# Performance work log

Measured on AMD Instinct MI355X. Metric: run time of the kernel, lower is better.

## Reference

```python
import jax, jax.numpy as jnp
import numpy as np

N, B, D, K, H = 30000, 16, 32, 8, 8
DIST = 5.0
EPS = 1e-6


def setup_inputs() -> dict:
    key = jax.random.key(0)
    ks = jax.random.split(key, 16)
    sc = 1.0 / np.sqrt(D)
    inp = {
        'pos': jax.random.uniform(ks[0], (N, 3), jnp.float32) * 20.0,
        'node_features': jax.random.normal(ks[1], (N, D), jnp.float32),
        'batch': jnp.sort(jax.random.randint(ks[2], (N,), 0, B, dtype=jnp.int32)),
        'bessel_weights': jnp.linspace(jnp.pi, K * jnp.pi, K).astype(jnp.float32),
        'init_dummy': jax.random.normal(ks[3], (D,), jnp.float32),
        'Wq_dummy': jax.random.normal(ks[4], (D, D), jnp.float32) * sc,
        'Wq_graph': jax.random.normal(ks[5], (D, D), jnp.float32) * sc,
        'Wdot': jax.random.normal(ks[6], (D, D), jnp.float32) * sc,
        'W1_kd': jax.random.normal(ks[7], (K, H), jnp.float32) / np.sqrt(K),
        'W2_kd': jax.random.normal(ks[8], (H, D * D), jnp.float32) / np.sqrt(H),
        'W1_vd': jax.random.normal(ks[9], (K, H), jnp.float32) / np.sqrt(K),
        'W2_vd': jax.random.normal(ks[10], (H, D * D), jnp.float32) / np.sqrt(H),
        'W1_kg': jax.random.normal(ks[11], (K, H), jnp.float32) / np.sqrt(K),
        'W2_kg': jax.random.normal(ks[12], (H, D * D), jnp.float32) / np.sqrt(H),
        'W1_vg': jax.random.normal(ks[13], (K, H), jnp.float32) / np.sqrt(K),
        'W2_vg': jax.random.normal(ks[14], (H, D * D), jnp.float32) / np.sqrt(H),
    }
    return inp


def reference(pos, node_features, batch, bessel_weights, init_dummy,
              Wq_dummy, Wq_graph, Wdot,
              W1_kd, W2_kd, W1_vd, W2_vd, W1_kg, W2_kg, W1_vg, W2_vg):
    scale = 1.0 / np.sqrt(D)

    # --- dummy edge features: per-batch z extents + bessel basis ---
    z = pos[:, 2]                                            # [N]
    z_min = jax.ops.segment_min(z, batch, num_segments=B)    # [B]
    z_max = jax.ops.segment_max(z, batch, num_segments=B)    # [B]
    bot_len = z - z_min[batch] + DIST                        # [N]
    top_len = z_max[batch] + DIST - z                        # [N]

    def bessel(x):  # [N] -> [N,K]
        return jnp.sin(bessel_weights * x[:, None]) / (x[:, None] + EPS)

    edge = jnp.stack([bessel(bot_len), bessel(top_len)], axis=1)  # [N,2,K]

    # --- init dummy node features [B, 2, D] ---
    dummy = jnp.broadcast_to(init_dummy, (B, 2, D))

    def gen_w(W1, W2):  # conditional weight generator (silu MLP)
        return (jax.nn.silu(edge @ W1) @ W2).reshape(N, 2, D, D)

    # --- dummy nodes attend over graph nodes (segment softmax) ---
    wk = gen_w(W1_kd, W2_kd)                                 # [N,2,D,D]
    wv = gen_w(W1_vd, W2_vd)
    q = (dummy @ Wq_dummy)[batch]                            # [N,2,D]
    k = jnp.einsum('nd,nsde->nse', node_features, wk)        # [N,2,D]
    v = jnp.einsum('nd,nsde->nse', node_features, wv)
    s = jnp.einsum('nsq,qk,nsk->ns', q, Wdot, k) * scale     # [N,2]
    m = jax.ops.segment_max(s, batch, num_segments=B)
    e = jnp.exp(s - m[batch])
    zsum = jax.ops.segment_sum(e, batch, num_segments=B)
    attn = e / zsum[batch]                                   # [N,2]
    dummy_new = dummy + jax.ops.segment_sum(attn[..., None] * v, batch, num_segments=B)

    # --- graph nodes attend over (2) dummy nodes ---
    wkg = gen_w(W1_kg, W2_kg)
    wvg = gen_w(W1_vg, W2_vg)
    d_per = dummy_new[batch]                                 # [N,2,D]
    kg = jnp.einsum('nsd,nsde->nse', d_per, wkg)
    vg = jnp.einsum('nsd,nsde->nse', d_per, wvg)
    qg = node_features @ Wq_graph                            # [N,D]
    sg = jnp.einsum('nq,qk,nsk->ns', qg, Wdot, kg) * scale   # [N,2]
    ag = jax.nn.softmax(sg, axis=1)
    x_new = node_features + jnp.einsum('ns,nsd->nd', ag, vg)  # [N,D]
    return x_new
```

## Files before the change

kernel.cpp:

```cpp
#include <hip/hip_runtime.h>
#include <math.h>

#define NN 30000
#define BB 16
#define DD 32
#define KK 8
#define HH 8
#define DIST_C 5.0f
#define EPS_C 1e-6f
#define SCALE_C 0.17677669529663687f

#define WS_ZMIN 0
#define WS_ZMAX 16
#define WS_ZSUM 32
#define WS_QW   64
#define WS_PK   96
#define WS_WC   352
#define WS_T    1376
#define WS_AKG  9568
#define WS_AVG  17760

#define NPB 32

__device__ __forceinline__ unsigned fencode(float f) {
    unsigned u = __float_as_uint(f);
    return (u & 0x80000000u) ? ~u : (u | 0x80000000u);
}
__device__ __forceinline__ float fdecode(unsigned c) {
    return __uint_as_float((c & 0x80000000u) ? (c ^ 0x80000000u) : ~c);
}
__device__ __forceinline__ float silu(float x) { return x / (1.0f + expf(-x)); }

__device__ __forceinline__ void bessel_edges(float bw0, float x0, float x1, float edge[2][8]) {
    float xs[2]; xs[0] = x0; xs[1] = x1;
    #pragma unroll
    for (int s = 0; s < 2; ++s) {
        float x = xs[s];
        float inv = 1.0f / (x + EPS_C);
        float th = bw0 * x;
        float c2 = 2.0f * cosf(th);
        float skm1 = 0.0f;
        float sk = sinf(th);
        #pragma unroll
        for (int k = 0; k < 8; ++k) {
            edge[s][k] = sk * inv;
            float nx = c2 * sk - skm1;
            skm1 = sk;
            sk = nx;
        }
    }
}

__global__ __launch_bounds__(256) void k_init(const float* __restrict__ init_dummy,
                                              const float* __restrict__ Wq_dummy,
                                              const float* __restrict__ Wdot,
                                              const float* __restrict__ W2_kd,
                                              const float* __restrict__ Wq_graph,
                                              float* __restrict__ ws) {
    __shared__ float qvec[32];
    __shared__ float qWl[32];
    int t = threadIdx.x;
    unsigned* wsu = (unsigned*)ws;
    if (t < 16) { wsu[WS_ZMIN + t] = 0xFFFFFFFFu; wsu[WS_ZMAX + t] = 0u; }
    if (t < 32) ws[WS_ZSUM + t] = 0.0f;
    for (int i = t; i < 8192; i += 256) ws[WS_T + i] = 0.0f;
    if (t < 32) {
        float acc = 0.0f;
        for (int d = 0; d < 32; ++d) acc += init_dummy[d] * Wq_dummy[d * 32 + t];
        qvec[t] = acc;
    }
    __syncthreads();
    if (t < 32) {
        float acc = 0.0f;
        for (int e = 0; e < 32; ++e) acc += qvec[e] * Wdot[e * 32 + t];
        qWl[t] = acc;
        ws[WS_QW + t] = acc;
    }
    __syncthreads();
    {
        int h = t >> 5, d = t & 31;
        float acc = 0.0f;
        for (int e = 0; e < 32; ++e) acc += W2_kd[h * 1024 + d * 32 + e] * qWl[e];
        ws[WS_PK + t] = acc;
    }
    for (int i = t; i < 1024; i += 256) {
        int d = i >> 5, e = i & 31;
        float acc = 0.0f;
        for (int m = 0; m < 32; ++m) acc += Wq_graph[d * 32 + m] * Wdot[m * 32 + e];
        ws[WS_WC + i] = acc;
    }
}

__global__ __launch_bounds__(256) void k_zminmax(const float* __restrict__ pos,
                                                 const int* __restrict__ batch,
                                                 float* __restrict__ ws) {
    __shared__ unsigned zl[16], zh[16];
    int t = threadIdx.x;
    if (t < 16) { zl[t] = 0xFFFFFFFFu; zh[t] = 0u; }
    __syncthreads();
    int n = blockIdx.x * 256 + t;
    if (n < NN) {
        unsigned c = fencode(pos[3 * n + 2]);
        int b = batch[n];
        atomicMin(&zl[b], c);
        atomicMax(&zh[b], c);
    }
    __syncthreads();
    unsigned* wsu = (unsigned*)ws;
    if (t < 16) {
        if (zl[t] != 0xFFFFFFFFu) atomicMin(&wsu[WS_ZMIN + t], zl[t]);
        if (zh[t] != 0u)          atomicMax(&wsu[WS_ZMAX + t], zh[t]);
    }
}

__global__ __launch_bounds__(256) void k_phase1(const float* __restrict__ pos,
                                                const int* __restrict__ batch,
                                                const float* __restrict__ nf,
                                                const float* __restrict__ bw,
                                                const float* __restrict__ W1_kd,
                                                const float* __restrict__ W1_vd,
                                                float* __restrict__ ws) {
    __shared__ __align__(16) float Fl[NPB * 36];
    __shared__ float Lw[NPB * 17];
    __shared__ int   Lb[NPB];
    __shared__ __align__(16) float Pk[256];
    __shared__ float W1kd[64], W1vd[64], zsl[32];
    int t = threadIdx.x;
    if (t < 64) { W1kd[t] = W1_kd[t]; W1vd[t] = W1_vd[t]; }
    Pk[t] = ws[WS_PK + t];
    if (t < 32) zsl[t] = 0.0f;

    int li = t >> 3, g = t & 7;
    int n0 = blockIdx.x * NPB;
    int n = n0 + li;
    bool valid = n < NN;
    float4 fv4 = make_float4(0.f, 0.f, 0.f, 0.f);
    int b = 0;
    if (valid) {
        b = batch[n];
        fv4 = ((const float4*)nf)[n * 8 + g];
        ((float4*)(Fl + li * 36))[g] = fv4;
        if (g == 0) Lb[li] = b;
    } else {
        if (g == 0) Lb[li] = -1;
    }
    __syncthreads();

    if (valid) {
        const unsigned* wsu = (const unsigned*)ws;
        float z = pos[3 * n + 2];
        float zmin = fdecode(wsu[WS_ZMIN + b]);
        float zmax = fdecode(wsu[WS_ZMAX + b]);
        float edge[2][8];
        bessel_edges(bw[0], z - zmin + DIST_C, zmax + DIST_C - z, edge);

        float up[8];
        const float4* Pk4 = (const float4*)Pk;
        #pragma unroll
        for (int h = 0; h < 8; ++h) {
            float4 p = Pk4[h * 8 + g];
            up[h] = fv4.x * p.x + fv4.y * p.y + fv4.z * p.z + fv4.w * p.w;
        }
        float kd0, kd1;
        {
            float p0 = 0.f, p1 = 0.f;
            #pragma unroll
            for (int k = 0; k < 8; ++k) {
                float w = W1kd[k * 8 + g];
                p0 += edge[0][k] * w;
                p1 += edge[1][k] * w;
            }
            kd0 = silu(p0); kd1 = silu(p1);
        }
        int lanebase = (t & 63) & 56;
        float sp0 = 0.f, sp1 = 0.f;
        #pragma unroll
        for (int h = 0; h < 8; ++h) {
            float a0 = __shfl(kd0, lanebase + h, 64);
            float a1 = __shfl(kd1, lanebase + h, 64);
            sp0 += a0 * up[h];
            sp1 += a1 * up[h];
        }
        #pragma unroll
        for (int m = 1; m < 8; m <<= 1) {
            sp0 += __shfl_xor(sp0, m, 64);
            sp1 += __shfl_xor(sp1, m, 64);
        }
        float ev0 = expf(sp0 * SCALE_C);
        float ev1 = expf(sp1 * SCALE_C);
        if (g == 0) {
            atomicAdd(&zsl[b * 2 + 0], ev0);
            atomicAdd(&zsl[b * 2 + 1], ev1);
        }
        float q0 = 0.f, q1 = 0.f;
        #pragma unroll
        for (int k = 0; k < 8; ++k) {
            float w = W1vd[k * 8 + g];
            q0 += edge[0][k] * w;
            q1 += edge[1][k] * w;
        }
        Lw[li * 17 + g]     = ev0 * silu(q0);
        Lw[li * 17 + 8 + g] = ev1 * silu(q1);
    }
    __syncthreads();
    if (t < 32 && zsl[t] != 0.0f) atomicAdd(&ws[WS_ZSUM + t], zsl[t]);

    int count = NN - n0; if (count > NPB) count = NPB;
    int bf = Lb[0], bl = Lb[count - 1];
    int sh = t & 15, dp = t >> 4;
    for (int b2 = bf; b2 <= bl; ++b2) {
        float a0 = 0.f, a1 = 0.f;
        for (int i = 0; i < count; ++i) {
            if (Lb[i] != b2) continue;
            float w = Lw[i * 17 + sh];
            float2 x = *(const float2*)(Fl + i * 36 + 2 * dp);
            a0 += w * x.x;
            a1 += w * x.y;
        }
        float* Tb = ws + WS_T + b2 * 512 + sh * 32 + 2 * dp;
        atomicAdd(&Tb[0], a0);
        atomicAdd(&Tb[1], a1);
    }
}

__global__ __launch_bounds__(256) void k_batch(const float* __restrict__ init_dummy,
                                               const float* __restrict__ W2_vd,
                                               const float* __restrict__ W2_kg,
                                               const float* __restrict__ W2_vg,
                                               float* __restrict__ ws) {
    int bs = blockIdx.x;
    int b = bs >> 1, s = bs & 1;
    int t = threadIdx.x;
    __shared__ float Tl[256];
    __shared__ float part[256];
    __shared__ float dn[32];
    Tl[t] = ws[WS_T + b * 512 + s * 256 + t];
    __syncthreads();
    {
        int h = t >> 5, e = t & 31;
        float acc = 0.0f;
        #pragma unroll
        for (int d = 0; d < 32; ++d) acc += Tl[h * 32 + d] * W2_vd[h * 1024 + d * 32 + e];
        part[t] = acc;
    }
    __syncthreads();
    if (t < 32) {
        float acc = 0.0f;
        #pragma unroll
        for (int h = 0; h < 8; ++h) acc += part[h * 32 + t];
        float zs = ws[WS_ZSUM + b * 2 + s];
        dn[t] = init_dummy[t] + acc / zs;
    }
    __syncthreads();
    {
        int h = t >> 5, e = t & 31;
        float ak = 0.0f, av = 0.0f;
        #pragma unroll
        for (int d = 0; d < 32; ++d) {
            float dv = dn[d];
            ak += dv * W2_kg[h * 1024 + d * 32 + e];
            av += dv * W2_vg[h * 1024 + d * 32 + e];
        }
        ws[WS_AKG + b * 512 + s * 256 + t] = ak;
        ws[WS_AVG + b * 512 + s * 256 + t] = av;
    }
}

__global__ __launch_bounds__(256) void k_final(const float* __restrict__ pos,
                                               const int* __restrict__ batch,
                                               const float* __restrict__ nf,
                                               const float* __restrict__ bw,
                                               const float* __restrict__ W1_kg,
                                               const float* __restrict__ W1_vg,
                                               const float* __restrict__ ws,
                                               float* __restrict__ out) {
    __shared__ __align__(16) float Wc[1024];
    __shared__ __align__(16) float Fl[NPB * 36];
    __shared__ float W1kg[64], W1vg[64];
    int t = threadIdx.x;
    for (int i = t; i < 1024; i += 256) Wc[i] = ws[WS_WC + i];
    if (t < 64) { W1kg[t] = W1_kg[t]; W1vg[t] = W1_vg[t]; }

    int li = t >> 3, g = t & 7;
    int n0 = blockIdx.x * NPB;
    int n = n0 + li;
    bool valid = n < NN;
    float4 fv4 = make_float4(0.f, 0.f, 0.f, 0.f);
    if (valid) {
        fv4 = ((const float4*)nf)[n * 8 + g];
        ((float4*)(Fl + li * 36))[g] = fv4;
    }
    __syncthreads();
    if (!valid) return;

    int b = batch[n];
    const unsigned* wsu = (const unsigned*)ws;
    float z = pos[3 * n + 2];
    float zmin = fdecode(wsu[WS_ZMIN + b]);
    float zmax = fdecode(wsu[WS_ZMAX + b]);
    float edge[2][8];
    bessel_edges(bw[0], z - zmin + DIST_C, zmax + DIST_C - z, edge);

    float ak0, ak1, av0, av1;
    {
        float pk0 = 0.f, pk1 = 0.f, pv0 = 0.f, pv1 = 0.f;
        #pragma unroll
        for (int k = 0; k < 8; ++k) {
            float wk = W1kg[k * 8 + g];
            float wv = W1vg[k * 8 + g];
            pk0 += edge[0][k] * wk; pk1 += edge[1][k] * wk;
            pv0 += edge[0][k] * wv; pv1 += edge[1][k] * wv;
        }
        ak0 = silu(pk0); ak1 = silu(pk1);
        av0 = silu(pv0); av1 = silu(pv1);
    }

    float f[32];
    {
        const float4* myF4 = (const float4*)(Fl + li * 36);
        #pragma unroll
        for (int j = 0; j < 8; ++j) {
            float4 v = myF4[j];
            f[4 * j] = v.x; f[4 * j + 1] = v.y; f[4 * j + 2] = v.z; f[4 * j + 3] = v.w;
        }
    }
    float4 q4 = make_float4(0.f, 0.f, 0.f, 0.f);
    const float4* Wc4 = (const float4*)Wc;
    #pragma unroll
    for (int d = 0; d < 32; ++d) {
        float fd = f[d];
        float4 w = Wc4[d * 8 + g];
        q4.x += fd * w.x; q4.y += fd * w.y; q4.z += fd * w.z; q4.w += fd * w.w;
    }

    int lanebase = (t & 63) & 56;
    const float4* Ak4 = (const float4*)(ws + WS_AKG);
    const float4* Av4 = (const float4*)(ws + WS_AVG);
    float p0 = 0.f, p1 = 0.f;
    #pragma unroll
    for (int h = 0; h < 8; ++h) {
        float4 a0 = Ak4[b * 128 + h * 8 + g];
        float4 a1 = Ak4[b * 128 + 64 + h * 8 + g];
        float d0 = q4.x * a0.x + q4.y * a0.y + q4.z * a0.z + q4.w * a0.w;
        float d1 = q4.x * a1.x + q4.y * a1.y + q4.z * a1.z + q4.w * a1.w;
        p0 += __shfl(ak0, lanebase + h, 64) * d0;
        p1 += __shfl(ak1, lanebase + h, 64) * d1;
    }
    #pragma unroll
    for (int m = 1; m < 8; m <<= 1) {
        p0 += __shfl_xor(p0, m, 64);
        p1 += __shfl_xor(p1, m, 64);
    }
    float sg0 = p0 * SCALE_C, sg1 = p1 * SCALE_C;
    float mm = fmaxf(sg0, sg1);
    float e0 = expf(sg0 - mm), e1 = expf(sg1 - mm);
    float inv = 1.0f / (e0 + e1);
    float ag0 = e0 * inv, ag1 = e1 * inv;

    float4 x4 = fv4;
    #pragma unroll
    for (int h = 0; h < 8; ++h) {
        float w0 = ag0 * __shfl(av0, lanebase + h, 64);
        float w1 = ag1 * __shfl(av1, lanebase + h, 64);
        float4 a0 = Av4[b * 128 + h * 8 + g];
        float4 a1 = Av4[b * 128 + 64 + h * 8 + g];
        x4.x += w0 * a0.x + w1 * a1.x;
        x4.y += w0 * a0.y + w1 * a1.y;
        x4.z += w0 * a0.z + w1 * a1.z;
        x4.w += w0 * a0.w + w1 * a1.w;
    }
    ((float4*)out)[n * 8 + g] = x4;
}

extern "C" void kernel_launch(void* const* d_in, const int* in_sizes, int n_in,
                              void* d_out, int out_size, void* d_ws, size_t ws_size,
                              hipStream_t stream) {
    const float* pos        = (const float*)d_in[0];
    const float* nf         = (const float*)d_in[1];
    const int*   batch      = (const int*)d_in[2];
    const float* bw         = (const float*)d_in[3];
    const float* init_dummy = (const float*)d_in[4];
    const float* Wq_dummy   = (const float*)d_in[5];
    const float* Wq_graph   = (const float*)d_in[6];
    const float* Wdot       = (const float*)d_in[7];
    const float* W1_kd      = (const float*)d_in[8];
    const float* W2_kd      = (const float*)d_in[9];
    const float* W1_vd      = (const float*)d_in[10];
    const float* W2_vd      = (const float*)d_in[11];
    const float* W1_kg      = (const float*)d_in[12];
    const float* W2_kg      = (const float*)d_in[13];
    const float* W1_vg      = (const float*)d_in[14];
    const float* W2_vg      = (const float*)d_in[15];
    float* ws  = (float*)d_ws;
    float* out = (float*)d_out;

    int nblk1 = (NN + 255) / 256;
    int nblk8 = (NN + NPB - 1) / NPB;
    hipLaunchKernelGGL(k_init, dim3(1), dim3(256), 0, stream,
                       init_dummy, Wq_dummy, Wdot, W2_kd, Wq_graph, ws);
    hipLaunchKernelGGL(k_zminmax, dim3(nblk1), dim3(256), 0, stream, pos, batch, ws);
    hipLaunchKernelGGL(k_phase1, dim3(nblk8), dim3(256), 0, stream,
                       pos, batch, nf, bw, W1_kd, W1_vd, ws);
    hipLaunchKernelGGL(k_batch, dim3(32), dim3(256), 0, stream,
                       init_dummy, W2_vd, W2_kg, W2_vg, ws);
    hipLaunchKernelGGL(k_final, dim3(nblk8), dim3(256), 0, stream,
                       pos, batch, nf, bw, W1_kg, W1_vg, ws, out);
}
```

Baseline: 124.3 us.

## Fuse five kernels into one cooperative persistent kernel with grid syncs

Replaces the five separate launches (init, z min/max, phase1, per-batch, final) with a single cooperative kernel of 469 blocks, each handling two 32-node tiles, separated by grid-wide syncs. Node features, z, batch ids and bessel edges are computed once per block and kept in registers and shared memory across phases instead of being reloaded. The z min/max reduction now writes per-block partials that 16 blocks reduce, replacing global atomics. A multi-launch fallback using mode flags remains for when cooperative launch is unavailable. The cost is four grid barriers and higher register and LDS pressure per block.

```diff
diff --git a/kernel.cpp b/kernel.cpp
--- a/kernel.cpp
+++ b/kernel.cpp
@@ -1,26 +1,35 @@
 #include <hip/hip_runtime.h>
+#include <hip/hip_cooperative_groups.h>
 #include <math.h>
+
+namespace cg = cooperative_groups;
 
 #define NN 30000
 #define BB 16
-#define DD 32
-#define KK 8
-#define HH 8
 #define DIST_C 5.0f
 #define EPS_C 1e-6f
 #define SCALE_C 0.17677669529663687f
 
-#define WS_ZMIN 0
-#define WS_ZMAX 16
-#define WS_ZSUM 32
-#define WS_QW   64
-#define WS_PK   96
-#define WS_WC   352
-#define WS_T    1376
-#define WS_AKG  9568
-#define WS_AVG  17760
-
 #define NPB 32
+#define TPB 2
+#define GRID 469
+
+#define WS_ZMIN  0
+#define WS_ZMAX  16
+#define WS_ZSUM  32
+#define WS_PK    96
+#define WS_WC    352
+#define WS_T     1376
+#define WS_AKG   9568
+#define WS_AVG   17760
+#define WS_ZPART 25952
+
+#define M_PRE 1
+#define M_RED 2
+#define M_A   4
+#define M_B   8
+#define M_C   16
+#define M_ALL 31
 
 __device__ __forceinline__ unsigned fencode(float f) {
     unsigned u = __float_as_uint(f);
@@ -51,325 +60,317 @@
     }
 }
 
-__global__ __launch_bounds__(256) void k_init(const float* __restrict__ init_dummy,
-                                              const float* __restrict__ Wq_dummy,
-                                              const float* __restrict__ Wdot,
-                                              const float* __restrict__ W2_kd,
-                                              const float* __restrict__ Wq_graph,
-                                              float* __restrict__ ws) {
-    __shared__ float qvec[32];
-    __shared__ float qWl[32];
+__global__ __launch_bounds__(256, 2) void k_main(
+    const float* __restrict__ pos, const int* __restrict__ batch,
+    const float* __restrict__ nf, const float* __restrict__ bw,
+    const float* __restrict__ W1_kd, const float* __restrict__ W1_vd,
+    const float* __restrict__ W1_kg, const float* __restrict__ W1_vg,
+    const float* __restrict__ init_dummy, const float* __restrict__ Wq_dummy,
+    const float* __restrict__ Wdot, const float* __restrict__ W2_kd,
+    const float* __restrict__ W2_vd, const float* __restrict__ W2_kg,
+    const float* __restrict__ W2_vg, const float* __restrict__ Wq_graph,
+    float* __restrict__ ws, float* __restrict__ out, int mode)
+{
+    __shared__ __align__(16) float Fl[TPB][NPB * 36];
+    __shared__ float Lw[TPB][NPB * 17];
+    __shared__ int   Lb[TPB][NPB];
+    __shared__ __align__(16) float Pk[256];
+    __shared__ __align__(16) float Wc[1024];
+    __shared__ float W1kd[64], W1vd[64], W1kg[64], W1vg[64], zsl[32];
+    __shared__ unsigned zl[16], zh[16];
+    __shared__ float qvec[32], qWl[32];
+    __shared__ float Tl[256], part[256], dn[32];
+
+    const bool coop   = (mode == M_ALL);
+    const bool do_pre = mode & M_PRE;
+    const bool do_red = mode & M_RED;
+    const bool do_a   = mode & M_A;
+    const bool do_b   = mode & M_B;
+    const bool do_c   = mode & M_C;
+
     int t = threadIdx.x;
+    int li = t >> 3, g = t & 7;
+    int lanebase = (t & 63) & 56;
     unsigned* wsu = (unsigned*)ws;
-    if (t < 16) { wsu[WS_ZMIN + t] = 0xFFFFFFFFu; wsu[WS_ZMAX + t] = 0u; }
-    if (t < 32) ws[WS_ZSUM + t] = 0.0f;
-    for (int i = t; i < 8192; i += 256) ws[WS_T + i] = 0.0f;
-    if (t < 32) {
-        float acc = 0.0f;
-        for (int d = 0; d < 32; ++d) acc += init_dummy[d] * Wq_dummy[d * 32 + t];
-        qvec[t] = acc;
-    }
-    __syncthreads();
-    if (t < 32) {
-        float acc = 0.0f;
-        for (int e = 0; e < 32; ++e) acc += qvec[e] * Wdot[e * 32 + t];
-        qWl[t] = acc;
-        ws[WS_QW + t] = acc;
-    }
-    __syncthreads();
-    {
-        int h = t >> 5, d = t & 31;
-        float acc = 0.0f;
-        for (int e = 0; e < 32; ++e) acc += W2_kd[h * 1024 + d * 32 + e] * qWl[e];
-        ws[WS_PK + t] = acc;
-    }
-    for (int i = t; i < 1024; i += 256) {
-        int d = i >> 5, e = i & 31;
-        float acc = 0.0f;
-        for (int m = 0; m < 32; ++m) acc += Wq_graph[d * 32 + m] * Wdot[m * 32 + e];
-        ws[WS_WC + i] = acc;
-    }
-}
-
-__global__ __launch_bounds__(256) void k_zminmax(const float* __restrict__ pos,
-                                                 const int* __restrict__ batch,
-                                                 float* __restrict__ ws) {
-    __shared__ unsigned zl[16], zh[16];
-    int t = threadIdx.x;
-    if (t < 16) { zl[t] = 0xFFFFFFFFu; zh[t] = 0u; }
-    __syncthreads();
-    int n = blockIdx.x * 256 + t;
-    if (n < NN) {
-        unsigned c = fencode(pos[3 * n + 2]);
-        int b = batch[n];
-        atomicMin(&zl[b], c);
-        atomicMax(&zh[b], c);
-    }
-    __syncthreads();
-    unsigned* wsu = (unsigned*)ws;
-    if (t < 16) {
-        if (zl[t] != 0xFFFFFFFFu) atomicMin(&wsu[WS_ZMIN + t], zl[t]);
-        if (zh[t] != 0u)          atomicMax(&wsu[WS_ZMAX + t], zh[t]);
-    }
-}
-
-__global__ __launch_bounds__(256) void k_phase1(const float* __restrict__ pos,
-                                                const int* __restrict__ batch,
-                                                const float* __restrict__ nf,
-                                                const float* __restrict__ bw,
-                                                const float* __restrict__ W1_kd,
-                                                const float* __restrict__ W1_vd,
-                                                float* __restrict__ ws) {
-    __shared__ __align__(16) float Fl[NPB * 36];
-    __shared__ float Lw[NPB * 17];
-    __shared__ int   Lb[NPB];
-    __shared__ __align__(16) float Pk[256];
-    __shared__ float W1kd[64], W1vd[64], zsl[32];
-    int t = threadIdx.x;
-    if (t < 64) { W1kd[t] = W1_kd[t]; W1vd[t] = W1_vd[t]; }
-    Pk[t] = ws[WS_PK + t];
-    if (t < 32) zsl[t] = 0.0f;
-
-    int li = t >> 3, g = t & 7;
-    int n0 = blockIdx.x * NPB;
-    int n = n0 + li;
-    bool valid = n < NN;
-    float4 fv4 = make_float4(0.f, 0.f, 0.f, 0.f);
-    int b = 0;
-    if (valid) {
-        b = batch[n];
-        fv4 = ((const float4*)nf)[n * 8 + g];
-        ((float4*)(Fl + li * 36))[g] = fv4;
-        if (g == 0) Lb[li] = b;
-    } else {
-        if (g == 0) Lb[li] = -1;
-    }
-    __syncthreads();
-
-    if (valid) {
-        const unsigned* wsu = (const unsigned*)ws;
-        float z = pos[3 * n + 2];
-        float zmin = fdecode(wsu[WS_ZMIN + b]);
-        float zmax = fdecode(wsu[WS_ZMAX + b]);
-        float edge[2][8];
-        bessel_edges(bw[0], z - zmin + DIST_C, zmax + DIST_C - z, edge);
-
-        float up[8];
-        const float4* Pk4 = (const float4*)Pk;
-        #pragma unroll
-        for (int h = 0; h < 8; ++h) {
-            float4 p = Pk4[h * 8 + g];
-            up[h] = fv4.x * p.x + fv4.y * p.y + fv4.z * p.z + fv4.w * p.w;
-        }
-        float kd0, kd1;
+
+    float4 fv4[TPB]; float zreg[TPB]; int bseg[TPB]; bool val[TPB];
+    float bw0 = 0.f;
+    if (do_pre || do_a || do_c) {
+        bw0 = bw[0];
+        #pragma unroll
+        for (int it = 0; it < TPB; ++it) {
+            int n = (blockIdx.x * TPB + it) * NPB + li;
+            val[it] = (n < NN);
+            bseg[it] = 0; zreg[it] = 0.f;
+            fv4[it] = make_float4(0.f, 0.f, 0.f, 0.f);
+            if (val[it]) {
+                bseg[it] = batch[n];
+                fv4[it] = ((const float4*)nf)[n * 8 + g];
+                ((float4*)(Fl[it] + li * 36))[g] = fv4[it];
+                zreg[it] = pos[3 * n + 2];
+                if (g == 0) Lb[it][li] = bseg[it];
+            } else if (g == 0) Lb[it][li] = -1;
+        }
+    }
+
+    if (do_pre) {
+        if (t < 16) { zl[t] = 0xFFFFFFFFu; zh[t] = 0u; }
+        __syncthreads();
+        #pragma unroll
+        for (int it = 0; it < TPB; ++it)
+            if (val[it] && g == 0) {
+                unsigned c = fencode(zreg[it]);
+                atomicMin(&zl[bseg[it]], c);
+                atomicMax(&zh[bseg[it]], c);
+            }
+        __syncthreads();
+        if (t < 16) {
+            wsu[WS_ZPART + blockIdx.x * 32 + t]      = zl[t];
+            wsu[WS_ZPART + blockIdx.x * 32 + 16 + t] = zh[t];
+        }
+        int xb = blockIdx.x;
+        if (xb >= 32 && xb < 48) {
+            int off = (xb - 32) * 512 + t;
+            ws[WS_T + off] = 0.f; ws[WS_T + off + 256] = 0.f;
+        } else if (xb == 48) {
+            if (t < 32) ws[WS_ZSUM + t] = 0.f;
+        } else if (xb == 49) {
+            if (t < 32) {
+                float acc = 0.f;
+                for (int d = 0; d < 32; ++d) acc += init_dummy[d] * Wq_dummy[d * 32 + t];
+                qvec[t] = acc;
+            }
+            __syncthreads();
+            if (t < 32) {
+                float acc = 0.f;
+                for (int e = 0; e < 32; ++e) acc += qvec[e] * Wdot[e * 32 + t];
+                qWl[t] = acc;
+            }
+            __syncthreads();
+            {
+                int h = t >> 5, d = t & 31;
+                float acc = 0.f;
+                for (int e = 0; e < 32; ++e) acc += W2_kd[h * 1024 + d * 32 + e] * qWl[e];
+                ws[WS_PK + t] = acc;
+            }
+        } else if (xb >= 50 && xb < 54) {
+            int i = (xb - 50) * 256 + t;
+            int d = i >> 5, e = i & 31;
+            float acc = 0.f;
+            for (int m = 0; m < 32; ++m) acc += Wq_graph[d * 32 + m] * Wdot[m * 32 + e];
+            ws[WS_WC + i] = acc;
+        }
+    }
+    if (coop) cg::this_grid().sync();
+
+    if (do_red && blockIdx.x < 16) {
+        int b = blockIdx.x;
+        unsigned mn = 0xFFFFFFFFu, mx = 0u;
+        for (int e = t; e < GRID; e += 256) {
+            unsigned a = wsu[WS_ZPART + e * 32 + b];
+            unsigned c = wsu[WS_ZPART + e * 32 + 16 + b];
+            mn = (a < mn) ? a : mn;
+            mx = (c > mx) ? c : mx;
+        }
+        if (t == 0) { zl[0] = 0xFFFFFFFFu; zh[0] = 0u; }
+        __syncthreads();
+        atomicMin(&zl[0], mn);
+        atomicMax(&zh[0], mx);
+        __syncthreads();
+        if (t == 0) { wsu[WS_ZMIN + b] = zl[0]; wsu[WS_ZMAX + b] = zh[0]; }
+    }
+    if (coop) cg::this_grid().sync();
+
+    float edge[TPB][2][8];
+    if (do_a || do_c) {
+        Pk[t] = ws[WS_PK + t];
+        for (int i = t; i < 1024; i += 256) Wc[i] = ws[WS_WC + i];
+        if (t < 64) { W1kd[t] = W1_kd[t]; W1vd[t] = W1_vd[t]; W1kg[t] = W1_kg[t]; W1vg[t] = W1_vg[t]; }
+        if (t < 32) zsl[t] = 0.f;
+        __syncthreads();
+        #pragma unroll
+        for (int it = 0; it < TPB; ++it)
+            if (val[it]) {
+                float zmin = fdecode(wsu[WS_ZMIN + bseg[it]]);
+                float zmax = fdecode(wsu[WS_ZMAX + bseg[it]]);
+                bessel_edges(bw0, zreg[it] - zmin + DIST_C, zmax + DIST_C - zreg[it], edge[it]);
+            }
+    }
+
+    if (do_a) {
+        #pragma unroll
+        for (int it = 0; it < TPB; ++it) {
+            if (val[it]) {
+                float up[8];
+                const float4* Pk4 = (const float4*)Pk;
+                #pragma unroll
+                for (int h = 0; h < 8; ++h) {
+                    float4 p = Pk4[h * 8 + g];
+                    up[h] = fv4[it].x * p.x + fv4[it].y * p.y + fv4[it].z * p.z + fv4[it].w * p.w;
+                }
+                float p0 = 0.f, p1 = 0.f;
+                #pragma unroll
+                for (int k = 0; k < 8; ++k) {
+                    float w = W1kd[k * 8 + g];
+                    p0 += edge[it][0][k] * w;
+                    p1 += edge[it][1][k] * w;
+                }
+                float kd0 = silu(p0), kd1 = silu(p1);
+                float sp0 = 0.f, sp1 = 0.f;
+                #pragma unroll
+                for (int h = 0; h < 8; ++h) {
+                    sp0 += __shfl(kd0, lanebase + h, 64) * up[h];
+                    sp1 += __shfl(kd1, lanebase + h, 64) * up[h];
+                }
+                #pragma unroll
+                for (int m = 1; m < 8; m <<= 1) {
+                    sp0 += __shfl_xor(sp0, m, 64);
+                    sp1 += __shfl_xor(sp1, m, 64);
+                }
+                float ev0 = expf(sp0 * SCALE_C);
+                float ev1 = expf(sp1 * SCALE_C);
+                if (g == 0) {
+                    atomicAdd(&zsl[bseg[it] * 2 + 0], ev0);
+                    atomicAdd(&zsl[bseg[it] * 2 + 1], ev1);
+                }
+                float q0 = 0.f, q1 = 0.f;
+                #pragma unroll
+                for (int k = 0; k < 8; ++k) {
+                    float w = W1vd[k * 8 + g];
+                    q0 += edge[it][0][k] * w;
+                    q1 += edge[it][1][k] * w;
+                }
+                Lw[it][li * 17 + g]     = ev0 * silu(q0);
+                Lw[it][li * 17 + 8 + g] = ev1 * silu(q1);
+            }
+        }
+        __syncthreads();
+        if (t < 32 && zsl[t] != 0.f) atomicAdd(&ws[WS_ZSUM + t], zsl[t]);
+        #pragma unroll
+        for (int it = 0; it < TPB; ++it) {
+            int n0 = (blockIdx.x * TPB + it) * NPB;
+            int count = NN - n0; if (count > NPB) count = NPB;
+            int bf = Lb[it][0], bl = Lb[it][count - 1];
+            int sh = t & 15, dp = t >> 4;
+            for (int b2 = bf; b2 <= bl; ++b2) {
+                float a0 = 0.f, a1 = 0.f;
+                for (int i = 0; i < count; ++i) {
+                    if (Lb[it][i] != b2) continue;
+                    float w = Lw[it][i * 17 + sh];
+                    float2 x = *(const float2*)(Fl[it] + i * 36 + 2 * dp);
+                    a0 += w * x.x;
+                    a1 += w * x.y;
+                }
+                float* Tb = ws + WS_T + b2 * 512 + sh * 32 + 2 * dp;
+                atomicAdd(&Tb[0], a0);
+                atomicAdd(&Tb[1], a1);
+            }
+        }
+    }
+    if (coop) cg::this_grid().sync();
+
+    if (do_b && blockIdx.x < 32) {
+        int bb = blockIdx.x >> 1, s = blockIdx.x & 1;
+        Tl[t] = ws[WS_T + bb * 512 + s * 256 + t];
+        __syncthreads();
         {
-            float p0 = 0.f, p1 = 0.f;
+            int h = t >> 5, e = t & 31;
+            float acc = 0.f;
             #pragma unroll
-            for (int k = 0; k < 8; ++k) {
-                float w = W1kd[k * 8 + g];
-                p0 += edge[0][k] * w;
-                p1 += edge[1][k] * w;
-            }
-            kd0 = silu(p0); kd1 = silu(p1);
-        }
-        int lanebase = (t & 63) & 56;
-        float sp0 = 0.f, sp1 = 0.f;
-        #pragma unroll
-        for (int h = 0; h < 8; ++h) {
-            float a0 = __shfl(kd0, lanebase + h, 64);
-            float a1 = __shfl(kd1, lanebase + h, 64);
-            sp0 += a0 * up[h];
-            sp1 += a1 * up[h];
-        }
-        #pragma unroll
-        for (int m = 1; m < 8; m <<= 1) {
-            sp0 += __shfl_xor(sp0, m, 64);
-            sp1 += __shfl_xor(sp1, m, 64);
-        }
-        float ev0 = expf(sp0 * SCALE_C);
-        float ev1 = expf(sp1 * SCALE_C);
-        if (g == 0) {
-            atomicAdd(&zsl[b * 2 + 0], ev0);
-            atomicAdd(&zsl[b * 2 + 1], ev1);
-        }
-        float q0 = 0.f, q1 = 0.f;
-        #pragma unroll
-        for (int k = 0; k < 8; ++k) {
-            float w = W1vd[k * 8 + g];
-            q0 += edge[0][k] * w;
-            q1 += edge[1][k] * w;
-        }
-        Lw[li * 17 + g]     = ev0 * silu(q0);
-        Lw[li * 17 + 8 + g] = ev1 * silu(q1);
-    }
-    __syncthreads();
-    if (t < 32 && zsl[t] != 0.0f) atomicAdd(&ws[WS_ZSUM + t], zsl[t]);
-
-    int count = NN - n0; if (count > NPB) count = NPB;
-    int bf = Lb[0], bl = Lb[count - 1];
-    int sh = t & 15, dp = t >> 4;
-    for (int b2 = bf; b2 <= bl; ++b2) {
-        float a0 = 0.f, a1 = 0.f;
-        for (int i = 0; i < count; ++i) {
-            if (Lb[i] != b2) continue;
-            float w = Lw[i * 17 + sh];
-            float2 x = *(const float2*)(Fl + i * 36 + 2 * dp);
-            a0 += w * x.x;
-            a1 += w * x.y;
-        }
-        float* Tb = ws + WS_T + b2 * 512 + sh * 32 + 2 * dp;
-        atomicAdd(&Tb[0], a0);
-        atomicAdd(&Tb[1], a1);
-    }
-}
-
-__global__ __launch_bounds__(256) void k_batch(const float* __restrict__ init_dummy,
-                                               const float* __restrict__ W2_vd,
-                                               const float* __restrict__ W2_kg,
-                                               const float* __restrict__ W2_vg,
-                                               float* __restrict__ ws) {
-    int bs = blockIdx.x;
-    int b = bs >> 1, s = bs & 1;
-    int t = threadIdx.x;
-    __shared__ float Tl[256];
-    __shared__ float part[256];
-    __shared__ float dn[32];
-    Tl[t] = ws[WS_T + b * 512 + s * 256 + t];
-    __syncthreads();
-    {
-        int h = t >> 5, e = t & 31;
-        float acc = 0.0f;
-        #pragma unroll
-        for (int d = 0; d < 32; ++d) acc += Tl[h * 32 + d] * W2_vd[h * 1024 + d * 32 + e];
-        part[t] = acc;
-    }
-    __syncthreads();
-    if (t < 32) {
-        float acc = 0.0f;
-        #pragma unroll
-        for (int h = 0; h < 8; ++h) acc += part[h * 32 + t];
-        float zs = ws[WS_ZSUM + b * 2 + s];
-        dn[t] = init_dummy[t] + acc / zs;
-    }
-    __syncthreads();
-    {
-        int h = t >> 5, e = t & 31;
-        float ak = 0.0f, av = 0.0f;
-        #pragma unroll
-        for (int d = 0; d < 32; ++d) {
-            float dv = dn[d];
-            ak += dv * W2_kg[h * 1024 + d * 32 + e];
-            av += dv * W2_vg[h * 1024 + d * 32 + e];
-        }
-        ws[WS_AKG + b * 512 + s * 256 + t] = ak;
-        ws[WS_AVG + b * 512 + s * 256 + t] = av;
-    }
-}
-
-__global__ __launch_bounds__(256) void k_final(const float* __restrict__ pos,
-                                               const int* __restrict__ batch,
-                                               const float* __restrict__ nf,
-                                               const float* __restrict__ bw,
-                                               const float* __restrict__ W1_kg,
-                                               const float* __restrict__ W1_vg,
-                                               const float* __restrict__ ws,
-                                               float* __restrict__ out) {
-    __shared__ __align__(16) float Wc[1024];
-    __shared__ __align__(16) float Fl[NPB * 36];
-    __shared__ float W1kg[64], W1vg[64];
-    int t = threadIdx.x;
-    for (int i = t; i < 1024; i += 256) Wc[i] = ws[WS_WC + i];
-    if (t < 64) { W1kg[t] = W1_kg[t]; W1vg[t] = W1_vg[t]; }
-
-    int li = t >> 3, g = t & 7;
-    int n0 = blockIdx.x * NPB;
-    int n = n0 + li;
-    bool valid = n < NN;
-    float4 fv4 = make_float4(0.f, 0.f, 0.f, 0.f);
-    if (valid) {
-        fv4 = ((const float4*)nf)[n * 8 + g];
-        ((float4*)(Fl + li * 36))[g] = fv4;
-    }
-    __syncthreads();
-    if (!valid) return;
-
-    int b = batch[n];
-    const unsigned* wsu = (const unsigned*)ws;
-    float z = pos[3 * n + 2];
-    float zmin = fdecode(wsu[WS_ZMIN + b]);
-    float zmax = fdecode(wsu[WS_ZMAX + b]);
-    float edge[2][8];
-    bessel_edges(bw[0], z - zmin + DIST_C, zmax + DIST_C - z, edge);
-
-    float ak0, ak1, av0, av1;
-    {
-        float pk0 = 0.f, pk1 = 0.f, pv0 = 0.f, pv1 = 0.f;
-        #pragma unroll
-        for (int k = 0; k < 8; ++k) {
-            float wk = W1kg[k * 8 + g];
-            float wv = W1vg[k * 8 + g];
-            pk0 += edge[0][k] * wk; pk1 += edge[1][k] * wk;
-            pv0 += edge[0][k] * wv; pv1 += edge[1][k] * wv;
-        }
-        ak0 = silu(pk0); ak1 = silu(pk1);
-        av0 = silu(pv0); av1 = silu(pv1);
-    }
-
-    float f[32];
-    {
-        const float4* myF4 = (const float4*)(Fl + li * 36);
-        #pragma unroll
-        for (int j = 0; j < 8; ++j) {
-            float4 v = myF4[j];
-            f[4 * j] = v.x; f[4 * j + 1] = v.y; f[4 * j + 2] = v.z; f[4 * j + 3] = v.w;
-        }
-    }
-    float4 q4 = make_float4(0.f, 0.f, 0.f, 0.f);
-    const float4* Wc4 = (const float4*)Wc;
-    #pragma unroll
-    for (int d = 0; d < 32; ++d) {
-        float fd = f[d];
-        float4 w = Wc4[d * 8 + g];
-        q4.x += fd * w.x; q4.y += fd * w.y; q4.z += fd * w.z; q4.w += fd * w.w;
-    }
-
-    int lanebase = (t & 63) & 56;
-    const float4* Ak4 = (const float4*)(ws + WS_AKG);
-    const float4* Av4 = (const float4*)(ws + WS_AVG);
-    float p0 = 0.f, p1 = 0.f;
-    #pragma unroll
-    for (int h = 0; h < 8; ++h) {
-        float4 a0 = Ak4[b * 128 + h * 8 + g];
-        float4 a1 = Ak4[b * 128 + 64 + h * 8 + g];
-        float d0 = q4.x * a0.x + q4.y * a0.y + q4.z * a0.z + q4.w * a0.w;
-        float d1 = q4.x * a1.x + q4.y * a1.y + q4.z * a1.z + q4.w * a1.w;
-        p0 += __shfl(ak0, lanebase + h, 64) * d0;
-        p1 += __shfl(ak1, lanebase + h, 64) * d1;
-    }
-    #pragma unroll
-    for (int m = 1; m < 8; m <<= 1) {
-        p0 += __shfl_xor(p0, m, 64);
-        p1 += __shfl_xor(p1, m, 64);
-    }
-    float sg0 = p0 * SCALE_C, sg1 = p1 * SCALE_C;
-    float mm = fmaxf(sg0, sg1);
-    float e0 = expf(sg0 - mm), e1 = expf(sg1 - mm);
-    float inv = 1.0f / (e0 + e1);
-    float ag0 = e0 * inv, ag1 = e1 * inv;
-
-    float4 x4 = fv4;
-    #pragma unroll
-    for (int h = 0; h < 8; ++h) {
-        float w0 = ag0 * __shfl(av0, lanebase + h, 64);
-        float w1 = ag1 * __shfl(av1, lanebase + h, 64);
-        float4 a0 = Av4[b * 128 + h * 8 + g];
-        float4 a1 = Av4[b * 128 + 64 + h * 8 + g];
-        x4.x += w0 * a0.x + w1 * a1.x;
-        x4.y += w0 * a0.y + w1 * a1.y;
-        x4.z += w0 * a0.z + w1 * a1.z;
-        x4.w += w0 * a0.w + w1 * a1.w;
-    }
-    ((float4*)out)[n * 8 + g] = x4;
+            for (int d = 0; d < 32; ++d) acc += Tl[h * 32 + d] * W2_vd[h * 1024 + d * 32 + e];
+            part[t] = acc;
+        }
+        __syncthreads();
+        if (t < 32) {
+            float acc = 0.f;
+            #pragma unroll
+            for (int h = 0; h < 8; ++h) acc += part[h * 32 + t];
+            float zs = ws[WS_ZSUM + bb * 2 + s];
+            dn[t] = init_dummy[t] + acc / zs;
+        }
+        __syncthreads();
+        {
+            int h = t >> 5, e = t & 31;
+            float ak = 0.f, av = 0.f;
+            #pragma unroll
+            for (int d = 0; d < 32; ++d) {
+                float dv = dn[d];
+                ak += dv * W2_kg[h * 1024 + d * 32 + e];
+                av += dv * W2_vg[h * 1024 + d * 32 + e];
+            }
+            ws[WS_AKG + bb * 512 + s * 256 + t] = ak;
+            ws[WS_AVG + bb * 512 + s * 256 + t] = av;
+        }
+    }
+    if (coop) cg::this_grid().sync();
+
+    if (do_c) {
+        const float4* Ak4 = (const float4*)(ws + WS_AKG);
+        const float4* Av4 = (const float4*)(ws + WS_AVG);
+        const float4* Wc4 = (const float4*)Wc;
+        #pragma unroll
+        for (int it = 0; it < TPB; ++it) {
+            if (val[it]) {
+                int b = bseg[it];
+                float ak0, ak1, av0, av1;
+                {
+                    float pk0 = 0.f, pk1 = 0.f, pv0 = 0.f, pv1 = 0.f;
+                    #pragma unroll
+                    for (int k = 0; k < 8; ++k) {
+                        float wk = W1kg[k * 8 + g];
+                        float wv = W1vg[k * 8 + g];
+                        pk0 += edge[it][0][k] * wk; pk1 += edge[it][1][k] * wk;
+                        pv0 += edge[it][0][k] * wv; pv1 += edge[it][1][k] * wv;
+                    }
+                    ak0 = silu(pk0); ak1 = silu(pk1);
+                    av0 = silu(pv0); av1 = silu(pv1);
+                }
+                float4 q4 = make_float4(0.f, 0.f, 0.f, 0.f);
+                const float* myF = Fl[it] + li * 36;
+                #pragma unroll
+                for (int d = 0; d < 32; ++d) {
+                    float fd = myF[d];
+                    float4 w = Wc4[d * 8 + g];
+                    q4.x += fd * w.x; q4.y += fd * w.y; q4.z += fd * w.z; q4.w += fd * w.w;
+                }
+                float p0 = 0.f, p1 = 0.f;
+                #pragma unroll
+                for (int h = 0; h < 8; ++h) {
+                    float4 a0 = Ak4[b * 128 + h * 8 + g];
+                    float4 a1 = Ak4[b * 128 + 64 + h * 8 + g];
+                    float d0 = q4.x * a0.x + q4.y * a0.y + q4.z * a0.z + q4.w * a0.w;
+                    float d1 = q4.x * a1.x + q4.y * a1.y + q4.z * a1.z + q4.w * a1.w;
+                    p0 += __shfl(ak0, lanebase + h, 64) * d0;
+                    p1 += __shfl(ak1, lanebase + h, 64) * d1;
+                }
+                #pragma unroll
+                for (int m = 1; m < 8; m <<= 1) {
+                    p0 += __shfl_xor(p0, m, 64);
+                    p1 += __shfl_xor(p1, m, 64);
+                }
+                float sg0 = p0 * SCALE_C, sg1 = p1 * SCALE_C;
+                float mm = fmaxf(sg0, sg1);
+                float e0 = expf(sg0 - mm), e1 = expf(sg1 - mm);
+                float inv = 1.0f / (e0 + e1);
+                float ag0 = e0 * inv, ag1 = e1 * inv;
+
+                float4 x4 = fv4[it];
+                #pragma unroll
+                for (int h = 0; h < 8; ++h) {
+                    float w0 = ag0 * __shfl(av0, lanebase + h, 64);
+                    float w1 = ag1 * __shfl(av1, lanebase + h, 64);
+                    float4 a0 = Av4[b * 128 + h * 8 + g];
+                    float4 a1 = Av4[b * 128 + 64 + h * 8 + g];
+                    x4.x += w0 * a0.x + w1 * a1.x;
+                    x4.y += w0 * a0.y + w1 * a1.y;
+                    x4.z += w0 * a0.z + w1 * a1.z;
+                    x4.w += w0 * a0.w + w1 * a1.w;
+                }
+                int n = (blockIdx.x * TPB + it) * NPB + li;
+                ((float4*)out)[n * 8 + g] = x4;
+            }
+        }
+    }
 }
 
 extern "C" void kernel_launch(void* const* d_in, const int* in_sizes, int n_in,
@@ -394,15 +395,51 @@
     float* ws  = (float*)d_ws;
     float* out = (float*)d_out;
 
-    int nblk1 = (NN + 255) / 256;
-    int nblk8 = (NN + NPB - 1) / NPB;
-    hipLaunchKernelGGL(k_init, dim3(1), dim3(256), 0, stream,
-                       init_dummy, Wq_dummy, Wdot, W2_kd, Wq_graph, ws);
-    hipLaunchKernelGGL(k_zminmax, dim3(nblk1), dim3(256), 0, stream, pos, batch, ws);
-    hipLaunchKernelGGL(k_phase1, dim3(nblk8), dim3(256), 0, stream,
-                       pos, batch, nf, bw, W1_kd, W1_vd, ws);
-    hipLaunchKernelGGL(k_batch, dim3(32), dim3(256), 0, stream,
-                       init_dummy, W2_vd, W2_kg, W2_vg, ws);
-    hipLaunchKernelGGL(k_final, dim3(nblk8), dim3(256), 0, stream,
-                       pos, batch, nf, bw, W1_kg, W1_vg, ws, out);
+    static int coop_ok = -1;
+    if (coop_ok < 0) {
+        int dev = 0;
+        (void)hipGetDevice(&dev);
+        int attr = 0;
+        (void)hipDeviceGetAttribute(&attr, hipDeviceAttributeCooperativeLaunch, dev);
+        int maxb = 0;
+        (void)hipOccupancyMaxActiveBlocksPerMultiprocessor(
+            &maxb, reinterpret_cast<const void*>(&k_main), 256, 0);
+        hipDeviceProp_t prop;
+        (void)hipGetDeviceProperties(&prop, dev);
+        coop_ok = (attr != 0 && maxb * prop.multiProcessorCount >= GRID) ? 1 : 0;
+    }
+
+    if (coop_ok == 1) {
+        int mode = M_ALL;
+        void* args[] = { (void*)&pos, (void*)&batch, (void*)&nf, (void*)&bw,
+                         (void*)&W1_kd, (void*)&W1_vd, (void*)&W1_kg, (void*)&W1_vg,
+                         (void*)&init_dummy, (void*)&Wq_dummy, (void*)&Wdot, (void*)&W2_kd,
+                         (void*)&W2_vd, (void*)&W2_kg, (void*)&W2_vg, (void*)&Wq_graph,
+                         (void*)&ws, (void*)&out, (void*)&mode };
+        hipError_t err = hipLaunchCooperativeKernel((const void*)k_main, dim3(GRID), dim3(256),
+                                                    args, 0, stream);
+        if (err == hipSuccess) return;
+        coop_ok = 0;
+    }
+
+    hipLaunchKernelGGL(k_main, dim3(GRID), dim3(256), 0, stream,
+                       pos, batch, nf, bw, W1_kd, W1_vd, W1_kg, W1_vg,
+                       init_dummy, Wq_dummy, Wdot, W2_kd, W2_vd, W2_kg, W2_vg, Wq_graph,
+                       ws, out, M_PRE);
+    hipLaunchKernelGGL(k_main, dim3(16), dim3(256), 0, stream,
+                       pos, batch, nf, bw, W1_kd, W1_vd, W1_kg, W1_vg,
+                       init_dummy, Wq_dummy, Wdot, W2_kd, W2_vd, W2_kg, W2_vg, Wq_graph,
+                       ws, out, M_RED);
+    hipLaunchKernelGGL(k_main, dim3(GRID), dim3(256), 0, stream,
+                       pos, batch, nf, bw, W1_kd, W1_vd, W1_kg, W1_vg,
+                       init_dummy, Wq_dummy, Wdot, W2_kd, W2_vd, W2_kg, W2_vg, Wq_graph,
+                       ws, out, M_A);
+    hipLaunchKernelGGL(k_main, dim3(32), dim3(256), 0, stream,
+                       pos, batch, nf, bw, W1_kd, W1_vd, W1_kg, W1_vg,
+                       init_dummy, Wq_dummy, Wdot, W2_kd, W2_vd, W2_kg, W2_vg, Wq_graph,
+                       ws, out, M_B);
+    hipLaunchKernelGGL(k_main, dim3(GRID), dim3(256), 0, stream,
+                       pos, batch, nf, bw, W1_kd, W1_vd, W1_kg, W1_vg,
+                       init_dummy, Wq_dummy, Wdot, W2_kd, W2_vd, W2_kg, W2_vg, Wq_graph,
+                       ws, out, M_C);
 }
```

Measured after the change: 142.0 us. +14.2%, slower.
